# Kernel optimization log

Measured on AMD Instinct MI355X. Metric: run time of the kernel, lower is better.

Reference implementation:

```python
import jax, jax.numpy as jnp
import numpy as np

S, B, MAX_IN, MAX_OUT = 2048, 32, 256, 80
MIN_IN = 20
EPS = 1e-5  # torch BatchNorm1d default


def setup_inputs() -> dict:
    key = jax.random.key(0)
    ks = jax.random.split(key, 4)
    # ragged gene-set sizes per subsystem, and DCell's output-size rule
    in_sizes = jax.random.randint(ks[0], (S,), MIN_IN, MAX_IN + 1)
    out_sizes = jnp.maximum(20, (0.3 * in_sizes).astype(jnp.int32))
    in_mask = (jnp.arange(MAX_IN)[None, :] < in_sizes[:, None]).astype(jnp.float32)   # [S, MAX_IN]
    out_mask = (jnp.arange(MAX_OUT)[None, :] < out_sizes[:, None]).astype(jnp.float32)  # [S, MAX_OUT]
    # gathered mutant states per subsystem (padded), [S, B, MAX_IN]
    x = jax.random.normal(ks[1], (S, B, MAX_IN), dtype=jnp.float32) * in_mask[:, None, :]
    # per-subsystem Linear params (stacked), Kaiming-ish scale
    W = jax.random.normal(ks[2], (S, MAX_OUT, MAX_IN), dtype=jnp.float32) / np.sqrt(MAX_IN).astype(np.float32)
    b = jax.random.normal(ks[3], (S, MAX_OUT), dtype=jnp.float32) * 0.01
    gamma = jnp.ones((S, MAX_OUT), dtype=jnp.float32)
    beta = jnp.zeros((S, MAX_OUT), dtype=jnp.float32)
    return {"x": x, "W": W, "b": b, "gamma": gamma, "beta": beta,
            "in_mask": in_mask, "out_mask": out_mask}


def reference(x, W, b, gamma, beta, in_mask, out_mask):
    # grouped Linear over all subsystems at once: [S,B,I] x [S,O,I] -> [S,B,O]
    xm = x * in_mask[:, None, :]
    h = jnp.einsum('sbi,soi->sbo', xm, W) + b[:, None, :]
    h = jnp.tanh(h)
    # BatchNorm1d (training mode): normalize over the batch dim per subsystem/feature
    mean = jnp.mean(h, axis=1, keepdims=True)
    var = jnp.mean(jnp.square(h - mean), axis=1, keepdims=True)  # biased, as torch BN uses
    y = (h - mean) * jax.lax.rsqrt(var + EPS) * gamma[:, None, :] + beta[:, None, :]
    # zero out padded output features
    return y * out_mask[:, None, :]
```

## Files before the change

### kernel.cpp

```cpp
#include <hip/hip_runtime.h>

#define S_TOT 2048
#define B_SZ  32
#define I_SZ  256
#define O_SZ  80

typedef _Float16 f16x8 __attribute__((ext_vector_type(8)));
typedef _Float16 f16x4 __attribute__((ext_vector_type(4)));
typedef float    f32x4 __attribute__((ext_vector_type(4)));

__global__ __launch_bounds__(320, 5) void dcell_kernel(
    const float* __restrict__ x,
    const float* __restrict__ W,
    const float* __restrict__ bias,
    const float* __restrict__ gamma,
    const float* __restrict__ beta,
    const float* __restrict__ in_mask,
    const float* __restrict__ out_mask,
    float* __restrict__ out)
{
  __shared__ char Xs[16384];

  const int s   = blockIdx.x;
  const int tid = threadIdx.x;

  const int w  = tid >> 6;
  const int l  = tid & 63;
  const int m  = l & 15;
  const int ks = l >> 4;
  const int ob = w * 16;
  const int o  = ob + m;
  const int swz = (m & 7) << 4;

  const float* im = in_mask + (size_t)s * I_SZ;
  float msum = im[0] + im[32] + im[64] + im[96] +
               im[128] + im[160] + im[192] + im[224];
  const int kcmax = (int)(msum + 0.5f);
  const int Kact  = kcmax * 32;

  const float* omp = out_mask + (size_t)s * O_SZ;
  float osum = omp[l] + ((l < 16) ? omp[64 + l] : 0.f);
#pragma unroll
  for (int d = 32; d; d >>= 1) osum += __shfl_xor(osum, d);
  const int out_sz = (int)(osum + 0.5f);
  const bool wave_act = (ob < out_sz);
  const bool lane_act = (o < out_sz);

  {
    const float* xg = x + (size_t)s * (B_SZ * I_SZ);
    for (int t = tid; t < (B_SZ * I_SZ) / 4; t += 320) {
      int flat = t * 4;
      int r = flat >> 8, c = flat & 255;
      if (c < Kact) {
        f32x4 v = *(const f32x4*)(xg + flat);
        int off = r * 512 + ((c * 2) ^ ((r & 7) << 4));
        f16x4 h;
        h[0] = (_Float16)v[0]; h[1] = (_Float16)v[1];
        h[2] = (_Float16)v[2]; h[3] = (_Float16)v[3];
        *(f16x4*)(Xs + off) = h;
      }
    }
  }

  f16x8 wf[8];
  {
    const float* wgp = W + ((size_t)s * O_SZ + o) * I_SZ + ks * 8;
#pragma unroll
    for (int kc = 0; kc < 8; ++kc) {
      if (kc < kcmax) {
        f16x8 h = {0, 0, 0, 0, 0, 0, 0, 0};
        if (lane_act) {
          f32x4 lo = *(const f32x4*)(wgp + kc * 32);
          f32x4 hi = *(const f32x4*)(wgp + kc * 32 + 4);
          h[0] = (_Float16)lo[0]; h[1] = (_Float16)lo[1];
          h[2] = (_Float16)lo[2]; h[3] = (_Float16)lo[3];
          h[4] = (_Float16)hi[0]; h[5] = (_Float16)hi[1];
          h[6] = (_Float16)hi[2]; h[7] = (_Float16)hi[3];
        }
        wf[kc] = h;
      }
    }
  }
  __syncthreads();

  float* og = out + (size_t)s * (B_SZ * O_SZ) + o;

  if (wave_act) {
    f32x4 acc0 = {0.f, 0.f, 0.f, 0.f};
    f32x4 acc1 = {0.f, 0.f, 0.f, 0.f};
    const char* xr0 = Xs + m * 512;
    const char* xr1 = Xs + (m + 16) * 512;
#pragma unroll
    for (int kc = 0; kc < 8; ++kc) {
      if (kc < kcmax) {
        int kb = (kc * 64 + ks * 16) ^ swz;
        f16x8 a0 = *(const f16x8*)(xr0 + kb);
        f16x8 a1 = *(const f16x8*)(xr1 + kb);
        acc0 = __builtin_amdgcn_mfma_f32_16x16x32_f16(a0, wf[kc], acc0, 0, 0, 0);
        acc1 = __builtin_amdgcn_mfma_f32_16x16x32_f16(a1, wf[kc], acc1, 0, 0, 0);
      }
    }

    const float bv = bias[s * O_SZ + o];
    float t0[4], t1[4];
    float sum = 0.f;
#pragma unroll
    for (int r = 0; r < 4; ++r) {
      t0[r] = tanhf(acc0[r] + bv);
      t1[r] = tanhf(acc1[r] + bv);
      sum += t0[r] + t1[r];
    }
    sum += __shfl_xor(sum, 16);
    sum += __shfl_xor(sum, 32);
    const float mean = sum * (1.0f / 32.0f);

    float vs = 0.f;
#pragma unroll
    for (int r = 0; r < 4; ++r) {
      float d0 = t0[r] - mean, d1 = t1[r] - mean;
      vs += d0 * d0 + d1 * d1;
    }
    vs += __shfl_xor(vs, 16);
    vs += __shfl_xor(vs, 32);
    const float rstd = rsqrtf(vs * (1.0f / 32.0f) + 1e-5f);

    const float g  = gamma[s * O_SZ + o] * rstd;
    const float be = beta[s * O_SZ + o];
    const float om = omp[o];

#pragma unroll
    for (int r = 0; r < 4; ++r) {
      int b0 = ks * 4 + r;
      og[(size_t)b0 * O_SZ]        = ((t0[r] - mean) * g + be) * om;
      og[(size_t)(b0 + 16) * O_SZ] = ((t1[r] - mean) * g + be) * om;
    }
  } else {
#pragma unroll
    for (int r = 0; r < 4; ++r) {
      int b0 = ks * 4 + r;
      og[(size_t)b0 * O_SZ]        = 0.f;
      og[(size_t)(b0 + 16) * O_SZ] = 0.f;
    }
  }
}

extern "C" void kernel_launch(void* const* d_in, const int* in_sizes, int n_in,
                              void* d_out, int out_size, void* d_ws, size_t ws_size,
                              hipStream_t stream) {
  const float* x        = (const float*)d_in[0];
  const float* W        = (const float*)d_in[1];
  const float* bias     = (const float*)d_in[2];
  const float* gamma    = (const float*)d_in[3];
  const float* beta     = (const float*)d_in[4];
  const float* in_mask  = (const float*)d_in[5];
  const float* out_mask = (const float*)d_in[6];
  float* out = (float*)d_out;

  dcell_kernel<<<dim3(S_TOT), dim3(320), 0, stream>>>(
      x, W, bias, gamma, beta, in_mask, out_mask, out);
}
```

Measured before the change: 29.37 us.

## Use fast tanh, wider x loads, earlier param loads, and raise occupancy hint

Replaces the library tanhf with an exp-based fast approximation and loads x as 8-wide float chunks converted to one f16x8 shared store per thread, with a fully unrolled fixed trip count. Bias, gamma, beta and the output mask are now loaded up front so their latency overlaps the GEMM, and the wave/lane activity test reads the out mask directly instead of doing a shuffle reduction. The launch bounds ask for 8 blocks per CU instead of 5, which may force register spilling. The fast tanh loses some accuracy near zero and large magnitudes.

```diff
diff --git a/kernel.cpp b/kernel.cpp
--- a/kernel.cpp
+++ b/kernel.cpp
@@ -6,10 +6,23 @@
 #define O_SZ  80
 
 typedef _Float16 f16x8 __attribute__((ext_vector_type(8)));
-typedef _Float16 f16x4 __attribute__((ext_vector_type(4)));
 typedef float    f32x4 __attribute__((ext_vector_type(4)));
 
-__global__ __launch_bounds__(320, 5) void dcell_kernel(
+__device__ __forceinline__ float ftanh(float v) {
+  float e = __expf(2.0f * v);
+  return 1.0f - __fdividef(2.0f, e + 1.0f);
+}
+
+__device__ __forceinline__ f16x8 cvt8(f32x4 lo, f32x4 hi) {
+  f16x8 h;
+  h[0] = (_Float16)lo[0]; h[1] = (_Float16)lo[1];
+  h[2] = (_Float16)lo[2]; h[3] = (_Float16)lo[3];
+  h[4] = (_Float16)hi[0]; h[5] = (_Float16)hi[1];
+  h[6] = (_Float16)hi[2]; h[7] = (_Float16)hi[3];
+  return h;
+}
+
+__global__ __launch_bounds__(320, 8) void dcell_kernel(
     const float* __restrict__ x,
     const float* __restrict__ W,
     const float* __restrict__ bias,
@@ -39,25 +52,35 @@
   const int Kact  = kcmax * 32;
 
   const float* omp = out_mask + (size_t)s * O_SZ;
-  float osum = omp[l] + ((l < 16) ? omp[64 + l] : 0.f);
-#pragma unroll
-  for (int d = 32; d; d >>= 1) osum += __shfl_xor(osum, d);
-  const int out_sz = (int)(osum + 0.5f);
-  const bool wave_act = (ob < out_sz);
-  const bool lane_act = (o < out_sz);
+  const bool wave_act = (omp[ob] != 0.0f);
+  const bool lane_act = (omp[o]  != 0.0f);
+
+  const float bv  = bias[s * O_SZ + o];
+  const float gm  = gamma[s * O_SZ + o];
+  const float be  = beta[s * O_SZ + o];
+  const float om  = omp[o];
 
   {
     const float* xg = x + (size_t)s * (B_SZ * I_SZ);
-    for (int t = tid; t < (B_SZ * I_SZ) / 4; t += 320) {
-      int flat = t * 4;
-      int r = flat >> 8, c = flat & 255;
+#pragma unroll
+    for (int i = 0; i < 3; ++i) {
+      int t = tid + i * 320;
+      int r = t >> 5, c = (t & 31) * 8;
       if (c < Kact) {
-        f32x4 v = *(const f32x4*)(xg + flat);
+        f32x4 lo = *(const f32x4*)(xg + t * 8);
+        f32x4 hi = *(const f32x4*)(xg + t * 8 + 4);
         int off = r * 512 + ((c * 2) ^ ((r & 7) << 4));
-        f16x4 h;
-        h[0] = (_Float16)v[0]; h[1] = (_Float16)v[1];
-        h[2] = (_Float16)v[2]; h[3] = (_Float16)v[3];
-        *(f16x4*)(Xs + off) = h;
+        *(f16x8*)(Xs + off) = cvt8(lo, hi);
+      }
+    }
+    if (tid < 64) {
+      int t = 960 + tid;
+      int r = t >> 5, c = (t & 31) * 8;
+      if (c < Kact) {
+        f32x4 lo = *(const f32x4*)(xg + t * 8);
+        f32x4 hi = *(const f32x4*)(xg + t * 8 + 4);
+        int off = r * 512 + ((c * 2) ^ ((r & 7) << 4));
+        *(f16x8*)(Xs + off) = cvt8(lo, hi);
       }
     }
   }
@@ -72,10 +95,7 @@
         if (lane_act) {
           f32x4 lo = *(const f32x4*)(wgp + kc * 32);
           f32x4 hi = *(const f32x4*)(wgp + kc * 32 + 4);
-          h[0] = (_Float16)lo[0]; h[1] = (_Float16)lo[1];
-          h[2] = (_Float16)lo[2]; h[3] = (_Float16)lo[3];
-          h[4] = (_Float16)hi[0]; h[5] = (_Float16)hi[1];
-          h[6] = (_Float16)hi[2]; h[7] = (_Float16)hi[3];
+          h = cvt8(lo, hi);
         }
         wf[kc] = h;
       }
@@ -101,13 +121,12 @@
       }
     }
 
-    const float bv = bias[s * O_SZ + o];
     float t0[4], t1[4];
     float sum = 0.f;
 #pragma unroll
     for (int r = 0; r < 4; ++r) {
-      t0[r] = tanhf(acc0[r] + bv);
-      t1[r] = tanhf(acc1[r] + bv);
+      t0[r] = ftanh(acc0[r] + bv);
+      t1[r] = ftanh(acc1[r] + bv);
       sum += t0[r] + t1[r];
     }
     sum += __shfl_xor(sum, 16);
@@ -124,9 +143,7 @@
     vs += __shfl_xor(vs, 32);
     const float rstd = rsqrtf(vs * (1.0f / 32.0f) + 1e-5f);
 
-    const float g  = gamma[s * O_SZ + o] * rstd;
-    const float be = beta[s * O_SZ + o];
-    const float om = omp[o];
+    const float g = gm * rstd;
 
 #pragma unroll
     for (int r = 0; r < 4; ++r) {
```

New measurement: 28.68 us, median of 2. 1.02x faster.
